# Kernel tuning notes

Hardware: AMD Instinct MI355X
Metric: run time of the kernel (lower is better)

Reference implementation:

```python
import jax, jax.numpy as jnp
import numpy as np

B, V, S, H = 16384, 16, 64, 512


def setup_inputs() -> dict:
    key = jax.random.key(0)
    kx, kw, kb, kws, kbs = jax.random.split(key, 5)
    x = jax.random.normal(kx, (B, V, S), dtype=jnp.float32)
    # per-variable linear layers: weight [V, S, H], bias [V, H]
    W = jax.random.normal(kw, (V, S, H), dtype=jnp.float32) * (1.0 / np.sqrt(S))
    b = jax.random.normal(kb, (V, H), dtype=jnp.float32) * 0.01
    # variable selection linear: hidden -> V
    W_sel = jax.random.normal(kws, (H, V), dtype=jnp.float32) * (1.0 / np.sqrt(H))
    b_sel = jax.random.normal(kbs, (V,), dtype=jnp.float32) * 0.01
    return {"x": x, "W": W, "b": b, "W_sel": W_sel, "b_sel": b_sel}


def reference(x, W, b, W_sel, b_sel):
    # per-variable linears: [B, V, H]
    transformed = jnp.einsum('bvs,vsh->bvh', x, W) + b  # grouped small GEMMs
    # torch stacks to [B, H, V]; mean over variable axis -> [B, H]
    flat = transformed.mean(axis=1)
    # softmax-gated selection weights [B, V] (dropout is identity in eval)
    weights = jax.nn.softmax(flat @ W_sel + b_sel, axis=-1)
    # weighted sum over variables -> [B, H]
    out = jnp.einsum('bvh,bv->bh', transformed, weights)
    return out
```

## Files before the change

### kernel.cpp

```cpp
#include <hip/hip_runtime.h>
#include <hip/hip_bf16.h>
#include <stdint.h>

#define B_ROWS 16384
#define VDIM   16
#define SDIM   64
#define HDIM   512
#define KDIM   1024
#define KP     1056
#define ASTR   1064
#define PLOG_OFF 136192
#define WLDS_OFF (136192 + 8704)
#define K2_LDS   (136192 + 8704 + 4096)

using bf16x8 = __attribute__((ext_vector_type(8))) __bf16;
using u16x8  = __attribute__((ext_vector_type(8))) unsigned short;
using f32x4  = __attribute__((ext_vector_type(4))) float;

__device__ __forceinline__ unsigned short f2bf(float f) {
  unsigned int u = __builtin_bit_cast(unsigned int, f);
  u = (u + 0x7FFFu + ((u >> 16) & 1u)) >> 16;
  return (unsigned short)u;
}
__device__ __forceinline__ float bf2f(unsigned short s) {
  return __builtin_bit_cast(float, (unsigned int)s << 16);
}

__global__ __launch_bounds__(256) void k0_prep(
    const float* __restrict__ W, const float* __restrict__ bias,
    const float* __restrict__ Wsel, const float* __restrict__ bsel,
    unsigned short* __restrict__ Bt, unsigned short* __restrict__ WcombT,
    float* __restrict__ bcomb) {
  __shared__ float bm[HDIM];
  __shared__ float part[16][17];
  const int t = threadIdx.x;
  if (blockIdx.x < 2112) {
    int idx = blockIdx.x * 256 + t;
    int k = idx >> 9;
    int n = idx & 511;
    float val;
    if (k < KDIM)            val = W[(size_t)k * HDIM + n];
    else if (k < KDIM + 16)  val = bias[(size_t)(k - KDIM) * HDIM + n];
    else                     val = 0.f;
    Bt[(size_t)n * KP + k] = f2bf(val);
    return;
  }
  const int bid = blockIdx.x - 2112;
  if (bid < 256) {
    const int wave = t >> 6, lane = t & 63;
    const int k = bid * 4 + wave;
    const float* wr = W + (size_t)k * HDIM;
    float s[16];
    #pragma unroll
    for (int v = 0; v < 16; ++v) s[v] = 0.f;
    #pragma unroll
    for (int j = 0; j < 8; ++j) {
      const int h = lane + 64 * j;
      const float a = wr[h];
      const float4* wl = (const float4*)(Wsel + h * 16);
      const float4 q0 = wl[0], q1 = wl[1], q2 = wl[2], q3 = wl[3];
      s[0]  = fmaf(a, q0.x, s[0]);  s[1]  = fmaf(a, q0.y, s[1]);
      s[2]  = fmaf(a, q0.z, s[2]);  s[3]  = fmaf(a, q0.w, s[3]);
      s[4]  = fmaf(a, q1.x, s[4]);  s[5]  = fmaf(a, q1.y, s[5]);
      s[6]  = fmaf(a, q1.z, s[6]);  s[7]  = fmaf(a, q1.w, s[7]);
      s[8]  = fmaf(a, q2.x, s[8]);  s[9]  = fmaf(a, q2.y, s[9]);
      s[10] = fmaf(a, q2.z, s[10]); s[11] = fmaf(a, q2.w, s[11]);
      s[12] = fmaf(a, q3.x, s[12]); s[13] = fmaf(a, q3.y, s[13]);
      s[14] = fmaf(a, q3.z, s[14]); s[15] = fmaf(a, q3.w, s[15]);
    }
    #pragma unroll
    for (int off = 32; off > 0; off >>= 1) {
      #pragma unroll
      for (int v = 0; v < 16; ++v) s[v] += __shfl_xor(s[v], off, 64);
    }
    float mine = 0.f;
    #pragma unroll
    for (int v = 0; v < 16; ++v) mine = (lane == v) ? s[v] : mine;
    if (lane < 16) WcombT[lane * KDIM + k] = f2bf(mine * (1.f / 16.f));
  } else {
    for (int h = t; h < HDIM; h += 256) {
      float s = 0.f;
      #pragma unroll
      for (int v = 0; v < VDIM; ++v) s += bias[v * HDIM + h];
      bm[h] = s * (1.f / 16.f);
    }
    __syncthreads();
    int v = t & 15, sl = t >> 4;
    float s = 0.f;
    for (int h = sl * 32; h < sl * 32 + 32; ++h) s = fmaf(bm[h], Wsel[h * VDIM + v], s);
    part[sl][v] = s;
    __syncthreads();
    if (t < 16) {
      float s2 = bsel[t];
      #pragma unroll
      for (int i = 0; i < 16; ++i) s2 += part[i][t];
      bcomb[t] = s2;
    }
  }
}

__global__ __launch_bounds__(512, 2) void k2f_fused(
    const float* __restrict__ x, const unsigned short* __restrict__ WcombT,
    const float* __restrict__ bcomb, const unsigned short* __restrict__ Bt,
    float* __restrict__ C) {
  extern __shared__ unsigned short As[];
  float* plog = (float*)((char*)As + PLOG_OFF);
  float* wlds = (float*)((char*)As + WLDS_OFF);

  const int t = threadIdx.x;
  const int rowb = blockIdx.x * 64;
  const int wave = t >> 6, lane = t & 63;
  const int mlane = lane & 15, quad = lane >> 4;

  const int srow = t >> 3;
  const int sc = (t & 7) * 8;
  u16x8 xreg[16];
  {
    const float* xr = x + (size_t)(rowb + srow) * KDIM + sc;
    unsigned short* aw = As + srow * ASTR + sc;
    #pragma unroll 4
    for (int i = 0; i < 16; ++i) {
      const float4 a0 = *(const float4*)(xr + i * 64);
      const float4 a1 = *(const float4*)(xr + i * 64 + 4);
      u16x8 u;
      u[0] = f2bf(a0.x); u[1] = f2bf(a0.y); u[2] = f2bf(a0.z); u[3] = f2bf(a0.w);
      u[4] = f2bf(a1.x); u[5] = f2bf(a1.y); u[6] = f2bf(a1.z); u[7] = f2bf(a1.w);
      xreg[i] = u;
      *(u16x8*)(aw + i * 64) = u;
    }
  }
  __syncthreads();

  {
    const int kh = wave >> 2, rg = wave & 3;
    const unsigned short* al = As + (rg * 16 + mlane) * ASTR + kh * 512 + quad * 8;
    const unsigned short* bl = WcombT + mlane * KDIM + kh * 512 + quad * 8;
    f32x4 acc = {0.f, 0.f, 0.f, 0.f};
    #pragma unroll
    for (int kt = 0; kt < 16; ++kt) {
      bf16x8 a = *(const bf16x8*)al; al += 32;
      bf16x8 b = *(const bf16x8*)bl; bl += 32;
      acc = __builtin_amdgcn_mfma_f32_16x16x32_bf16(a, b, acc, 0, 0, 0);
    }
    float* pl = plog + ((size_t)((kh * 4 + rg) * 16 + quad * 4) * 17 + mlane);
    #pragma unroll
    for (int r = 0; r < 4; ++r) pl[r * 17] = acc[r];
  }
  __syncthreads();

  if (t < 64) {
    const int rg = t >> 4, r = t & 15;
    const float* p0 = plog + ((size_t)(rg * 16 + r) * 17);
    const float* p1 = plog + ((size_t)((4 + rg) * 16 + r) * 17);
    float l[16];
    float mx = -1e30f;
    #pragma unroll
    for (int v = 0; v < 16; ++v) {
      l[v] = p0[v] + p1[v] + bcomb[v];
      mx = fmaxf(mx, l[v]);
    }
    float s = 0.f;
    #pragma unroll
    for (int v = 0; v < 16; ++v) { l[v] = __expf(l[v] - mx); s += l[v]; }
    const float inv = 1.f / s;
    float* wo = wlds + t * 16;
    #pragma unroll
    for (int v = 0; v < 16; ++v) wo[v] = l[v] * inv;
  }
  __syncthreads();

  {
    float wv[16];
    const float4* wq = (const float4*)(wlds + srow * 16);
    #pragma unroll
    for (int q = 0; q < 4; ++q) {
      const float4 f = wq[q];
      wv[4 * q + 0] = f.x; wv[4 * q + 1] = f.y; wv[4 * q + 2] = f.z; wv[4 * q + 3] = f.w;
    }
    unsigned short* aw = As + srow * ASTR + sc;
    #pragma unroll 4
    for (int i = 0; i < 16; ++i) {
      const float w = wv[i];
      const u16x8 a = xreg[i];
      u16x8 o;
      #pragma unroll
      for (int j = 0; j < 8; ++j) o[j] = f2bf(w * bf2f(a[j]));
      *(u16x8*)(aw + i * 64) = o;
    }
    if ((t & 7) < 4) {
      const int j8 = (t & 7) * 8;
      unsigned short o[8];
      #pragma unroll
      for (int jj = 0; jj < 8; ++jj)
        o[jj] = (j8 + jj < 16) ? f2bf(wv[j8 + jj]) : (unsigned short)0;
      *(u16x8*)(As + srow * ASTR + KDIM + j8) = *(const u16x8*)o;
    }
  }

  const int colb = wave * 64;
  const unsigned short* bp[4];
  #pragma unroll
  for (int j = 0; j < 4; ++j)
    bp[j] = Bt + (size_t)(colb + j * 16 + mlane) * KP + quad * 8;

  bf16x8 bv0[4], bv1[4];
  #pragma unroll
  for (int j = 0; j < 4; ++j) {
    bv0[j] = *(const bf16x8*)(bp[j]);
    bv1[j] = *(const bf16x8*)(bp[j] + 32);
    bp[j] += 64;
  }

  __syncthreads();

  const unsigned short* ap[4];
  #pragma unroll
  for (int i = 0; i < 4; ++i)
    ap[i] = As + (i * 16 + mlane) * ASTR + quad * 8;

  f32x4 acc[4][4];
  const f32x4 z = {0.f, 0.f, 0.f, 0.f};
  #pragma unroll
  for (int i = 0; i < 4; ++i)
    #pragma unroll
    for (int j = 0; j < 4; ++j) acc[i][j] = z;

  #pragma unroll 1
  for (int kt = 0; kt < 33; ++kt) {
    bf16x8 bnext[4];
    if (kt < 31) {
      #pragma unroll
      for (int j = 0; j < 4; ++j) { bnext[j] = *(const bf16x8*)bp[j]; bp[j] += 32; }
    }
    bf16x8 av[4];
    #pragma unroll
    for (int i = 0; i < 4; ++i) { av[i] = *(const bf16x8*)ap[i]; ap[i] += 32; }
    #pragma unroll
    for (int i = 0; i < 4; ++i)
      #pragma unroll
      for (int j = 0; j < 4; ++j)
        acc[i][j] = __builtin_amdgcn_mfma_f32_16x16x32_bf16(av[i], bv0[j], acc[i][j], 0, 0, 0);
    #pragma unroll
    for (int j = 0; j < 4; ++j) { bv0[j] = bv1[j]; bv1[j] = bnext[j]; }
  }

  #pragma unroll
  for (int i = 0; i < 4; ++i)
    #pragma unroll
    for (int j = 0; j < 4; ++j)
      #pragma unroll
      for (int r = 0; r < 4; ++r) {
        const size_t row = (size_t)rowb + i * 16 + quad * 4 + r;
        const int col = colb + j * 16 + mlane;
        C[row * HDIM + col] = acc[i][j][r];
      }
}

extern "C" void kernel_launch(void* const* d_in, const int* in_sizes, int n_in,
                              void* d_out, int out_size, void* d_ws, size_t ws_size,
                              hipStream_t stream) {
  const float* x    = (const float*)d_in[0];
  const float* W    = (const float*)d_in[1];
  const float* bias = (const float*)d_in[2];
  const float* Wsel = (const float*)d_in[3];
  const float* bsel = (const float*)d_in[4];
  float* out = (float*)d_out;

  char* ws = (char*)d_ws;
  unsigned short* Bt     = (unsigned short*)(ws);
  unsigned short* WcombT = (unsigned short*)(ws + 1081344);
  float*          bcomb  = (float*)(ws + 1114112);

  static int lds_set = 0;
  if (!lds_set) {
    hipFuncSetAttribute((const void*)k2f_fused,
                        hipFuncAttributeMaxDynamicSharedMemorySize, K2_LDS);
    lds_set = 1;
  }

  k0_prep<<<2369, 256, 0, stream>>>(W, bias, Wsel, bsel, Bt, WcombT, bcomb);
  k2f_fused<<<256, 512, K2_LDS, stream>>>(x, WcombT, bcomb, Bt, out);
}
```

Measured before the change: 151.5 us.

## Halve fused-kernel row tile, tile the weight transpose through LDS, add nontemporal I/O

The fused kernel now processes 32 rows per block instead of 64. That halves LDS use, doubles the grid to 512 blocks and raises the occupancy hint to 4 blocks per CU, so more of the GPU is filled and latency is better hidden. The prep kernel transposes W into bf16 using a 32x256 LDS tile, giving vectorized 16-byte stores instead of scattered 2-byte stores. Streaming loads of x and stores of C become nontemporal. The trade-off is that each block of Bt is now loaded twice as often relative to the MFMA work.

```diff
diff --git a/kernel.cpp b/kernel.cpp
--- a/kernel.cpp
+++ b/kernel.cpp
@@ -9,9 +9,10 @@
 #define KDIM   1024
 #define KP     1056
 #define ASTR   1064
-#define PLOG_OFF 136192
-#define WLDS_OFF (136192 + 8704)
-#define K2_LDS   (136192 + 8704 + 4096)
+#define MROWS  32
+#define PLOG_OFF 68096
+#define WLDS_OFF (68096 + 8704)
+#define K2_LDS   (68096 + 8704 + 2048)
 
 using bf16x8 = __attribute__((ext_vector_type(8))) __bf16;
 using u16x8  = __attribute__((ext_vector_type(8))) unsigned short;
@@ -33,19 +34,32 @@
     float* __restrict__ bcomb) {
   __shared__ float bm[HDIM];
   __shared__ float part[16][17];
+  __shared__ unsigned short tile[32][264];
   const int t = threadIdx.x;
-  if (blockIdx.x < 2112) {
-    int idx = blockIdx.x * 256 + t;
-    int k = idx >> 9;
-    int n = idx & 511;
-    float val;
-    if (k < KDIM)            val = W[(size_t)k * HDIM + n];
-    else if (k < KDIM + 16)  val = bias[(size_t)(k - KDIM) * HDIM + n];
-    else                     val = 0.f;
-    Bt[(size_t)n * KP + k] = f2bf(val);
+  if (blockIdx.x < 66) {
+    const int k0 = (blockIdx.x >> 1) * 32;
+    const int n  = ((blockIdx.x & 1) << 8) + t;
+    #pragma unroll 8
+    for (int kk = 0; kk < 32; ++kk) {
+      const int k = k0 + kk;
+      float val;
+      if (k < KDIM)            val = W[(size_t)k * HDIM + n];
+      else if (k < KDIM + 16)  val = bias[(size_t)(k - KDIM) * HDIM + n];
+      else                     val = 0.f;
+      tile[kk][t] = f2bf(val);
+    }
+    __syncthreads();
+    unsigned short* dst = Bt + (size_t)n * KP + k0;
+    #pragma unroll
+    for (int seg = 0; seg < 4; ++seg) {
+      unsigned short o[8];
+      #pragma unroll
+      for (int jj = 0; jj < 8; ++jj) o[jj] = tile[seg * 8 + jj][t];
+      *(u16x8*)(dst + seg * 8) = *(const u16x8*)o;
+    }
     return;
   }
-  const int bid = blockIdx.x - 2112;
+  const int bid = blockIdx.x - 66;
   if (bid < 256) {
     const int wave = t >> 6, lane = t & 63;
     const int k = bid * 4 + wave;
@@ -99,7 +113,7 @@
   }
 }
 
-__global__ __launch_bounds__(512, 2) void k2f_fused(
+__global__ __launch_bounds__(512, 4) void k2f_fused(
     const float* __restrict__ x, const unsigned short* __restrict__ WcombT,
     const float* __restrict__ bcomb, const unsigned short* __restrict__ Bt,
     float* __restrict__ C) {
@@ -108,56 +122,58 @@
   float* wlds = (float*)((char*)As + WLDS_OFF);
 
   const int t = threadIdx.x;
-  const int rowb = blockIdx.x * 64;
+  const int rowb = blockIdx.x * MROWS;
   const int wave = t >> 6, lane = t & 63;
   const int mlane = lane & 15, quad = lane >> 4;
 
-  const int srow = t >> 3;
-  const int sc = (t & 7) * 8;
-  u16x8 xreg[16];
+  const int srow = t >> 4;
+  const int sc = (t & 15) * 8;
+  u16x8 xreg[8];
   {
     const float* xr = x + (size_t)(rowb + srow) * KDIM + sc;
     unsigned short* aw = As + srow * ASTR + sc;
-    #pragma unroll 4
-    for (int i = 0; i < 16; ++i) {
-      const float4 a0 = *(const float4*)(xr + i * 64);
-      const float4 a1 = *(const float4*)(xr + i * 64 + 4);
+    #pragma unroll
+    for (int i = 0; i < 8; ++i) {
+      const f32x4 a0 = __builtin_nontemporal_load((const f32x4*)(xr + i * 128));
+      const f32x4 a1 = __builtin_nontemporal_load((const f32x4*)(xr + i * 128 + 4));
       u16x8 u;
-      u[0] = f2bf(a0.x); u[1] = f2bf(a0.y); u[2] = f2bf(a0.z); u[3] = f2bf(a0.w);
-      u[4] = f2bf(a1.x); u[5] = f2bf(a1.y); u[6] = f2bf(a1.z); u[7] = f2bf(a1.w);
+      u[0] = f2bf(a0[0]); u[1] = f2bf(a0[1]); u[2] = f2bf(a0[2]); u[3] = f2bf(a0[3]);
+      u[4] = f2bf(a1[0]); u[5] = f2bf(a1[1]); u[6] = f2bf(a1[2]); u[7] = f2bf(a1[3]);
       xreg[i] = u;
-      *(u16x8*)(aw + i * 64) = u;
+      *(u16x8*)(aw + i * 128) = u;
     }
   }
   __syncthreads();
 
   {
-    const int kh = wave >> 2, rg = wave & 3;
-    const unsigned short* al = As + (rg * 16 + mlane) * ASTR + kh * 512 + quad * 8;
-    const unsigned short* bl = WcombT + mlane * KDIM + kh * 512 + quad * 8;
+    const int kh = wave >> 1, rg = wave & 1;
+    const unsigned short* al = As + (rg * 16 + mlane) * ASTR + kh * 256 + quad * 8;
+    const unsigned short* bl = WcombT + mlane * KDIM + kh * 256 + quad * 8;
     f32x4 acc = {0.f, 0.f, 0.f, 0.f};
     #pragma unroll
-    for (int kt = 0; kt < 16; ++kt) {
+    for (int kt = 0; kt < 8; ++kt) {
       bf16x8 a = *(const bf16x8*)al; al += 32;
       bf16x8 b = *(const bf16x8*)bl; bl += 32;
       acc = __builtin_amdgcn_mfma_f32_16x16x32_bf16(a, b, acc, 0, 0, 0);
     }
-    float* pl = plog + ((size_t)((kh * 4 + rg) * 16 + quad * 4) * 17 + mlane);
+    float* pl = plog + ((size_t)((kh * 2 + rg) * 16 + quad * 4) * 17 + mlane);
     #pragma unroll
     for (int r = 0; r < 4; ++r) pl[r * 17] = acc[r];
   }
   __syncthreads();
 
-  if (t < 64) {
-    const int rg = t >> 4, r = t & 15;
-    const float* p0 = plog + ((size_t)(rg * 16 + r) * 17);
-    const float* p1 = plog + ((size_t)((4 + rg) * 16 + r) * 17);
+  if (t < 32) {
+    const int rg = t >> 4, rr = t & 15;
     float l[16];
     float mx = -1e30f;
     #pragma unroll
     for (int v = 0; v < 16; ++v) {
-      l[v] = p0[v] + p1[v] + bcomb[v];
-      mx = fmaxf(mx, l[v]);
+      float s = bcomb[v];
+      #pragma unroll
+      for (int kq = 0; kq < 4; ++kq)
+        s += plog[((size_t)((kq * 2 + rg) * 16 + rr)) * 17 + v];
+      l[v] = s;
+      mx = fmaxf(mx, s);
     }
     float s = 0.f;
     #pragma unroll
@@ -171,24 +187,26 @@
 
   {
     float wv[16];
-    const float4* wq = (const float4*)(wlds + srow * 16);
+    const f32x4* wq = (const f32x4*)(wlds + srow * 16);
     #pragma unroll
     for (int q = 0; q < 4; ++q) {
-      const float4 f = wq[q];
-      wv[4 * q + 0] = f.x; wv[4 * q + 1] = f.y; wv[4 * q + 2] = f.z; wv[4 * q + 3] = f.w;
-    }
+      const f32x4 f = wq[q];
+      wv[4 * q + 0] = f[0]; wv[4 * q + 1] = f[1];
+      wv[4 * q + 2] = f[2]; wv[4 * q + 3] = f[3];
+    }
+    const int vbase = (t & 15) >> 3;
     unsigned short* aw = As + srow * ASTR + sc;
-    #pragma unroll 4
-    for (int i = 0; i < 16; ++i) {
-      const float w = wv[i];
+    #pragma unroll
+    for (int i = 0; i < 8; ++i) {
+      const float w = wv[2 * i + vbase];
       const u16x8 a = xreg[i];
       u16x8 o;
       #pragma unroll
       for (int j = 0; j < 8; ++j) o[j] = f2bf(w * bf2f(a[j]));
-      *(u16x8*)(aw + i * 64) = o;
-    }
-    if ((t & 7) < 4) {
-      const int j8 = (t & 7) * 8;
+      *(u16x8*)(aw + i * 128) = o;
+    }
+    if ((t & 15) < 4) {
+      const int j8 = (t & 15) * 8;
       unsigned short o[8];
       #pragma unroll
       for (int jj = 0; jj < 8; ++jj)
@@ -213,15 +231,15 @@
 
   __syncthreads();
 
-  const unsigned short* ap[4];
-  #pragma unroll
-  for (int i = 0; i < 4; ++i)
+  const unsigned short* ap[2];
+  #pragma unroll
+  for (int i = 0; i < 2; ++i)
     ap[i] = As + (i * 16 + mlane) * ASTR + quad * 8;
 
-  f32x4 acc[4][4];
+  f32x4 acc[2][4];
   const f32x4 z = {0.f, 0.f, 0.f, 0.f};
   #pragma unroll
-  for (int i = 0; i < 4; ++i)
+  for (int i = 0; i < 2; ++i)
     #pragma unroll
     for (int j = 0; j < 4; ++j) acc[i][j] = z;
 
@@ -232,11 +250,11 @@
       #pragma unroll
       for (int j = 0; j < 4; ++j) { bnext[j] = *(const bf16x8*)bp[j]; bp[j] += 32; }
     }
-    bf16x8 av[4];
-    #pragma unroll
-    for (int i = 0; i < 4; ++i) { av[i] = *(const bf16x8*)ap[i]; ap[i] += 32; }
-    #pragma unroll
-    for (int i = 0; i < 4; ++i)
+    bf16x8 av[2];
+    #pragma unroll
+    for (int i = 0; i < 2; ++i) { av[i] = *(const bf16x8*)ap[i]; ap[i] += 32; }
+    #pragma unroll
+    for (int i = 0; i < 2; ++i)
       #pragma unroll
       for (int j = 0; j < 4; ++j)
         acc[i][j] = __builtin_amdgcn_mfma_f32_16x16x32_bf16(av[i], bv0[j], acc[i][j], 0, 0, 0);
@@ -245,14 +263,14 @@
   }
 
   #pragma unroll
-  for (int i = 0; i < 4; ++i)
+  for (int i = 0; i < 2; ++i)
     #pragma unroll
     for (int j = 0; j < 4; ++j)
       #pragma unroll
       for (int r = 0; r < 4; ++r) {
         const size_t row = (size_t)rowb + i * 16 + quad * 4 + r;
         const int col = colb + j * 16 + mlane;
-        C[row * HDIM + col] = acc[i][j][r];
+        __builtin_nontemporal_store(acc[i][j][r], &C[row * HDIM + col]);
       }
 }
 
@@ -278,6 +296,6 @@
     lds_set = 1;
   }
 
-  k0_prep<<<2369, 256, 0, stream>>>(W, bias, Wsel, bsel, Bt, WcombT, bcomb);
-  k2f_fused<<<256, 512, K2_LDS, stream>>>(x, WcombT, bcomb, Bt, out);
-}
+  k0_prep<<<323, 256, 0, stream>>>(W, bias, Wsel, bsel, Bt, WcombT, bcomb);
+  k2f_fused<<<512, 512, K2_LDS, stream>>>(x, WcombT, bcomb, Bt, out);
+}
```

Result: slower. 162.7 us (+7.4%).
